# Optimization experiments

Measured on AMD Instinct MI355X. Metric: run time of the kernel, lower is better.

Reference implementation:

```python
import jax, jax.numpy as jnp
import numpy as np

BATCH, INPUTDIM, OUTDIM, GRIDSIZE = 4096, 256, 256, 64


def setup_inputs() -> dict:
    key = jax.random.key(0)
    k1, k2 = jax.random.split(key)
    x = jax.random.normal(k1, (BATCH, INPUTDIM), dtype=jnp.float32)
    # xavier_uniform over (2, outdim, inputdim, gridsize): fan_in = inputdim*gridsize, fan_out = outdim*gridsize
    fan_in = INPUTDIM * GRIDSIZE
    fan_out = OUTDIM * GRIDSIZE
    limit = float(np.sqrt(6.0 / (fan_in + fan_out)))
    fouriercoeffs = jax.random.uniform(
        k2, (2, OUTDIM, INPUTDIM, GRIDSIZE), dtype=jnp.float32,
        minval=-limit, maxval=limit)
    bias = jnp.zeros((1, OUTDIM), dtype=jnp.float32)
    return {"x": x, "fouriercoeffs": fouriercoeffs, "bias": bias}


def reference(x, fouriercoeffs, bias):
    # x: [B, inputdim]; fouriercoeffs: [2, outdim, inputdim, gridsize]; bias: [1, outdim]
    # gridsize_param is clamp/round'ed to an int in torch -> static = initial_gridsize here.
    G = fouriercoeffs.shape[-1]
    k = jnp.arange(1, G + 1, dtype=x.dtype)        # [G] frequencies 1..G
    xk = x[:, :, None] * k                          # [B, inputdim, G]
    c = jnp.cos(xk)                                 # [B, inputdim, G]
    s = jnp.sin(xk)                                 # [B, inputdim, G]
    # Fused contraction over (inputdim, gridsize) -- avoids the naive
    # [B, outdim, inputdim, gridsize] broadcast tensor of the torch code.
    y = (jnp.einsum('big,oig->bo', c, fouriercoeffs[0])
         + jnp.einsum('big,oig->bo', s, fouriercoeffs[1])
         + bias)                                    # [B, outdim]
    return y
```

## Files before the change

### kernel.cpp

```cpp
#include <hip/hip_runtime.h>
#include <hip/hip_bf16.h>


typedef __attribute__((ext_vector_type(8))) short short8;
typedef __attribute__((ext_vector_type(4))) float f32x4;

#define SPLITK 8
#define ICHUNK (256 / SPLITK)

__device__ __forceinline__ unsigned short f2bf(float f) {
    unsigned u = __builtin_bit_cast(unsigned, f);
    u += 0x7fffu + ((u >> 16) & 1u);
    return (unsigned short)(u >> 16);
}
__device__ __forceinline__ unsigned pkbf16(float a, float b) {
    return (unsigned)f2bf(a) | ((unsigned)f2bf(b) << 16);
}

__device__ __forceinline__ unsigned pk_rh(float a, float b) {
    unsigned ua = __builtin_bit_cast(unsigned, a) + 0x8000u;
    unsigned ub = __builtin_bit_cast(unsigned, b) + 0x8000u;
    return __builtin_amdgcn_perm(ub, ua, 0x07060302u);
}

__device__ __forceinline__ void dbl2(float c, float s, float& co, float& so) {
    float t = c + c;
    co = __builtin_fmaf(t, c, -1.f);
    so = t * s;
}
__device__ __forceinline__ void rot2(float c, float s, float cr, float sr,
                                     float& co, float& so) {
    float t = s * sr;
    co = __builtin_fmaf(c, cr, -t);
    float u = s * cr;
    so = __builtin_fmaf(c, sr, u);
}

__device__ __forceinline__ short8 chain8(float m1, float fm1, float f0) {
    unsigned r[4];
    float vp = fm1, v = f0;
    #pragma unroll
    for (int h = 0; h < 4; ++h) {
        float v1 = __builtin_fmaf(m1, v, -vp);
        r[h] = pk_rh(v, v1);
        float v2 = __builtin_fmaf(m1, v1, -v);
        vp = v1; v = v2;
    }
    uint4 u; u.x = r[0]; u.y = r[1]; u.z = r[2]; u.w = r[3];
    return __builtin_bit_cast(short8, u);
}

__device__ __forceinline__ void async_load16(const void* g, void* l) {
    __builtin_amdgcn_global_load_lds(
        (const __attribute__((address_space(1))) unsigned int*)g,
        (__attribute__((address_space(3))) unsigned int*)l,
        16, 0, 0);
}

__global__ void init_out_kernel(float* __restrict__ out, const float* __restrict__ bias) {
    int tid = blockIdx.x * 256 + threadIdx.x;
    float4 b4 = ((const float4*)bias)[tid & 63];
    ((float4*)out)[tid] = b4;
}

__global__ __launch_bounds__(256) void convert_coeffs2(
    const float* __restrict__ fc, unsigned short* __restrict__ ws2)
{
    __shared__ unsigned short lsh[256 * 72];
    const int bx = blockIdx.x;
    const int i = bx >> 1, y = bx & 1;
    const int t = threadIdx.x;
    {
        const int tt = t >> 7, op = t & 127;
        const float4* src = (const float4*)(fc +
            ((((size_t)tt * 256) + y * 128 + op) * 256 + i) * 64);
        uint4* dst = (uint4*)(lsh + t * 72);
        #pragma unroll
        for (int q2 = 0; q2 < 8; ++q2) {
            float4 a = src[q2 * 2], b = src[q2 * 2 + 1];
            uint4 v;
            v.x = pkbf16(a.x, a.y); v.y = pkbf16(a.z, a.w);
            v.z = pkbf16(b.x, b.y); v.w = pkbf16(b.z, b.w);
            dst[q2] = v;
        }
    }
    __syncthreads();
    uint4* wdst = (uint4*)ws2 + (size_t)bx * 2048;
    #pragma unroll
    for (int rep = 0; rep < 8; ++rep) {
        int gi = rep * 256 + t;
        int sog = gi >> 6, ll = gi & 63;
        int s = sog >> 3, og = sog & 7;
        int op = og * 16 + (ll & 15);
        int k = s * 32 + ((ll >> 4) * 8);
        int tt = k >> 6, g0 = k & 63;
        wdst[gi] = *(const uint4*)(lsh + (tt * 128 + op) * 72 + g0);
    }
}

template <bool USE_WS>
__global__ __launch_bounds__(256, 2) void fkan_gemm(
    const float* __restrict__ x, const float* __restrict__ fc,
    const unsigned short* __restrict__ bws, float* __restrict__ out)
{
    __shared__ uint4 Bimg[2][2048];
    __shared__ float xs[ICHUNK][128];

    const int t  = threadIdx.x;
    const int l  = t & 63;
    const int w  = t >> 6;
    const int wr = w >> 1, wc = w & 1;
    const int q  = l >> 4;
    const int m  = l & 15;
    const int rowBase = blockIdx.x * 128;
    const int by      = blockIdx.y;
    const int colBase = by * 128;
    const int iBase   = blockIdx.z * ICHUNK;
    const float q8f   = (float)(q * 8);

    f32x4 acc[4][4];
    #pragma unroll
    for (int a = 0; a < 4; ++a)
        #pragma unroll
        for (int b = 0; b < 4; ++b) acc[a][b] = (f32x4)0.0f;

    auto stageB = [&](int p, int i) {
        if (USE_WS) {
            const unsigned short* base = bws + ((size_t)(i * 2 + by) * 2048) * 8;
            #pragma unroll
            for (int cc = 0; cc < 8; ++cc) {
                int c = cc * 4 + w;
                async_load16(base + (size_t)(c * 64 + l) * 8, (void*)(&Bimg[p][c * 64]));
            }
        } else {
            #pragma unroll
            for (int gg = 0; gg < 8; ++gg) {
                int gi  = gg * 256 + t;
                int sog = gi >> 6, ll = gi & 63;
                int s = sog >> 3, ogb = sog & 7;
                int o = ogb * 16 + (ll & 15);
                int k = s * 32 + (ll >> 4) * 8;
                int tt = k >> 6, g = k & 63;
                const float4* p4 = (const float4*)(fc +
                    ((((size_t)tt * 256 + colBase + o) * 256 + i) * 64 + g));
                float4 a = p4[0], b = p4[1];
                uint4 v;
                v.x = pkbf16(a.x, a.y); v.y = pkbf16(a.z, a.w);
                v.z = pkbf16(b.x, b.y); v.w = pkbf16(b.z, b.w);
                Bimg[p][gi] = v;
            }
        }
    };

    stageB(0, iBase);
    {
        int r = t >> 1, c0 = (t & 1) * 16;
        const float4* px = (const float4*)(x + (size_t)(rowBase + r) * 256 + iBase + c0);
        float4 v0 = px[0], v1 = px[1], v2 = px[2], v3 = px[3];
        float tmp[16] = { v0.x, v0.y, v0.z, v0.w, v1.x, v1.y, v1.z, v1.w,
                          v2.x, v2.y, v2.z, v2.w, v3.x, v3.y, v3.z, v3.w };
        #pragma unroll
        for (int j = 0; j < 16; ++j) xs[c0 + j][r] = tmp[j];
    }
    __syncthreads();

    #pragma unroll 1
    for (int ii = 0; ii < ICHUNK; ++ii) {
        const int p = ii & 1;

        short8 bF[4][4];
        #pragma unroll
        for (int s = 0; s < 4; ++s)
            #pragma unroll
            for (int cf = 0; cf < 4; ++cf)
                bF[s][cf] = __builtin_bit_cast(short8,
                    Bimg[p][(s * 8 + wc * 4 + cf) * 64 + l]);

        if (ii + 1 < ICHUNK) stageB(p ^ 1, iBase + ii + 1);

        short8 aF[4][4];
        #pragma unroll
        for (int rf = 0; rf < 4; ++rf) {
            float xv = xs[ii][wr * 64 + rf * 16 + m];
            float s1, c1;
            __sincosf(xv, &s1, &c1);
            const float m1 = c1 + c1;
            float c2, s2, c4, s4, c8, s8, c16, s16, c32, s32;
            dbl2(c1, s1, c2, s2);
            dbl2(c2, s2, c4, s4);
            dbl2(c4, s4, c8, s8);
            dbl2(c8, s8, c16, s16);
            dbl2(c16, s16, c32, s32);
            float c24, s24;
            rot2(c16, s16, c8, s8, c24, s24);
            float cq = (q == 0) ? 1.f : (q == 1) ? c8 : (q == 2) ? c16 : c24;
            float sq = (q == 0) ? 0.f : (q == 1) ? s8 : (q == 2) ? s16 : s24;
            float cq1, sq1, cB, sB, cB1, sB1;
            rot2(cq, sq, c1, s1, cq1, sq1);
            rot2(cq, sq, c32, s32, cB, sB);
            rot2(cB, sB, c1, s1, cB1, sB1);
            aF[rf][0] = chain8(m1, cq, cq1);
            aF[rf][1] = chain8(m1, cB, cB1);
            aF[rf][2] = chain8(m1, sq, sq1);
            aF[rf][3] = chain8(m1, sB, sB1);
        }

        #pragma unroll
        for (int s = 0; s < 4; ++s)
            #pragma unroll
            for (int rf = 0; rf < 4; ++rf)
                #pragma unroll
                for (int cf = 0; cf < 4; ++cf)
                    acc[rf][cf] = __builtin_amdgcn_mfma_f32_16x16x32_bf16(
                        aF[rf][s], bF[s][cf], acc[rf][cf], 0, 0, 0);

        __syncthreads();
    }

    const int lr = (l >> 4) * 4;
    const int r0 = rowBase + wr * 64 + lr;
    const int c0 = colBase + wc * 64 + m;
    #pragma unroll
    for (int rf = 0; rf < 4; ++rf)
        #pragma unroll
        for (int cf = 0; cf < 4; ++cf)
            #pragma unroll
            for (int e = 0; e < 4; ++e)
                atomicAdd(out + (size_t)(r0 + rf * 16 + e) * 256 + (c0 + cf * 16),
                          acc[rf][cf][e]);
}

extern "C" void kernel_launch(void* const* d_in, const int* in_sizes, int n_in,
                              void* d_out, int out_size, void* d_ws, size_t ws_size,
                              hipStream_t stream) {
    const float* x    = (const float*)d_in[0];
    const float* fc   = (const float*)d_in[1];
    const float* bias = (const float*)d_in[2];
    float* out = (float*)d_out;
    unsigned short* bws = (unsigned short*)d_ws;

    hipLaunchKernelGGL(init_out_kernel, dim3(1024), dim3(256), 0, stream, out, bias);

    const size_t wsNeed = (size_t)512 * 2048 * 16;
    if (ws_size >= wsNeed) {
        hipLaunchKernelGGL(convert_coeffs2, dim3(512), dim3(256), 0, stream, fc, bws);
        hipLaunchKernelGGL((fkan_gemm<true>), dim3(32, 2, SPLITK), dim3(256), 0, stream,
                           x, fc, bws, out);
    } else {
        hipLaunchKernelGGL((fkan_gemm<false>), dim3(32, 2, SPLITK), dim3(256), 0, stream,
                           x, fc, bws, out);
    }
}
```

Baseline: 182.7 us.

## Simplify coefficient conversion, use hardware bf16 packing and native sin/cos

The coefficient conversion kernel is rewritten to drop its LDS staging. Each thread now reads its 8 floats straight from global memory at the target layout, converts them and writes one 16-byte packed value, using 8x more blocks. bf16 packing uses the hardware cvt_pk_bf16_f32 builtin when available, which gives round-to-nearest-even instead of the previous round-half-up trick. In the main GEMM, __sincosf is replaced with the native v_sin/v_cos builtins on x/(2π), which drops range reduction and risks accuracy for large |x|. The strided global reads in conversion may coalesce worse than the previous staged version.

```diff
diff --git a/kernel.cpp b/kernel.cpp
--- a/kernel.cpp
+++ b/kernel.cpp
@@ -8,20 +8,21 @@
 #define SPLITK 8
 #define ICHUNK (256 / SPLITK)
 
-__device__ __forceinline__ unsigned short f2bf(float f) {
-    unsigned u = __builtin_bit_cast(unsigned, f);
-    u += 0x7fffu + ((u >> 16) & 1u);
-    return (unsigned short)(u >> 16);
-}
+#define INV2PI 0.15915494309189535f
+
+#if __has_builtin(__builtin_amdgcn_cvt_pk_bf16_f32)
+typedef __attribute__((ext_vector_type(2))) __bf16 bf16x2_t;
 __device__ __forceinline__ unsigned pkbf16(float a, float b) {
-    return (unsigned)f2bf(a) | ((unsigned)f2bf(b) << 16);
-}
-
-__device__ __forceinline__ unsigned pk_rh(float a, float b) {
+    bf16x2_t v = __builtin_amdgcn_cvt_pk_bf16_f32(a, b);
+    return __builtin_bit_cast(unsigned, v);
+}
+#else
+__device__ __forceinline__ unsigned pkbf16(float a, float b) {
     unsigned ua = __builtin_bit_cast(unsigned, a) + 0x8000u;
     unsigned ub = __builtin_bit_cast(unsigned, b) + 0x8000u;
     return __builtin_amdgcn_perm(ub, ua, 0x07060302u);
 }
+#endif
 
 __device__ __forceinline__ void dbl2(float c, float s, float& co, float& so) {
     float t = c + c;
@@ -42,7 +43,7 @@
     #pragma unroll
     for (int h = 0; h < 4; ++h) {
         float v1 = __builtin_fmaf(m1, v, -vp);
-        r[h] = pk_rh(v, v1);
+        r[h] = pkbf16(v, v1);
         float v2 = __builtin_fmaf(m1, v1, -v);
         vp = v1; v = v2;
     }
@@ -63,39 +64,24 @@
     ((float4*)out)[tid] = b4;
 }
 
-__global__ __launch_bounds__(256) void convert_coeffs2(
+__global__ __launch_bounds__(256) void convert_coeffs3(
     const float* __restrict__ fc, unsigned short* __restrict__ ws2)
 {
-    __shared__ unsigned short lsh[256 * 72];
-    const int bx = blockIdx.x;
-    const int i = bx >> 1, y = bx & 1;
-    const int t = threadIdx.x;
-    {
-        const int tt = t >> 7, op = t & 127;
-        const float4* src = (const float4*)(fc +
-            ((((size_t)tt * 256) + y * 128 + op) * 256 + i) * 64);
-        uint4* dst = (uint4*)(lsh + t * 72);
-        #pragma unroll
-        for (int q2 = 0; q2 < 8; ++q2) {
-            float4 a = src[q2 * 2], b = src[q2 * 2 + 1];
-            uint4 v;
-            v.x = pkbf16(a.x, a.y); v.y = pkbf16(a.z, a.w);
-            v.z = pkbf16(b.x, b.y); v.w = pkbf16(b.z, b.w);
-            dst[q2] = v;
-        }
-    }
-    __syncthreads();
-    uint4* wdst = (uint4*)ws2 + (size_t)bx * 2048;
-    #pragma unroll
-    for (int rep = 0; rep < 8; ++rep) {
-        int gi = rep * 256 + t;
-        int sog = gi >> 6, ll = gi & 63;
-        int s = sog >> 3, og = sog & 7;
-        int op = og * 16 + (ll & 15);
-        int k = s * 32 + ((ll >> 4) * 8);
-        int tt = k >> 6, g0 = k & 63;
-        wdst[gi] = *(const uint4*)(lsh + (tt * 128 + op) * 72 + g0);
-    }
+    unsigned flat = blockIdx.x * 256 + threadIdx.x;
+    unsigned bx = flat >> 11, gi = flat & 2047;
+    unsigned i = bx >> 1, y = bx & 1;
+    unsigned sog = gi >> 6, ll = gi & 63;
+    unsigned s = sog >> 3, og = sog & 7;
+    unsigned op = og * 16 + (ll & 15);
+    unsigned k = s * 32 + ((ll >> 4) * 8);
+    unsigned tt = k >> 6, g0 = k & 63;
+    const float4* src = (const float4*)(fc +
+        ((((size_t)tt * 256 + y * 128 + op) * 256 + i) * 64 + g0));
+    float4 a = src[0], b = src[1];
+    uint4 v;
+    v.x = pkbf16(a.x, a.y); v.y = pkbf16(a.z, a.w);
+    v.z = pkbf16(b.x, b.y); v.w = pkbf16(b.z, b.w);
+    ((uint4*)ws2)[flat] = v;
 }
 
 template <bool USE_WS>
@@ -116,7 +102,6 @@
     const int by      = blockIdx.y;
     const int colBase = by * 128;
     const int iBase   = blockIdx.z * ICHUNK;
-    const float q8f   = (float)(q * 8);
 
     f32x4 acc[4][4];
     #pragma unroll
@@ -182,8 +167,9 @@
         #pragma unroll
         for (int rf = 0; rf < 4; ++rf) {
             float xv = xs[ii][wr * 64 + rf * 16 + m];
-            float s1, c1;
-            __sincosf(xv, &s1, &c1);
+            float rev = xv * INV2PI;
+            float s1 = __builtin_amdgcn_sinf(rev);
+            float c1 = __builtin_amdgcn_cosf(rev);
             const float m1 = c1 + c1;
             float c2, s2, c4, s4, c8, s8, c16, s16, c32, s32;
             dbl2(c1, s1, c2, s2);
@@ -243,7 +229,7 @@
 
     const size_t wsNeed = (size_t)512 * 2048 * 16;
     if (ws_size >= wsNeed) {
-        hipLaunchKernelGGL(convert_coeffs2, dim3(512), dim3(256), 0, stream, fc, bws);
+        hipLaunchKernelGGL(convert_coeffs3, dim3(4096), dim3(256), 0, stream, fc, bws);
         hipLaunchKernelGGL((fkan_gemm<true>), dim3(32, 2, SPLITK), dim3(256), 0, stream,
                            x, fc, bws, out);
     } else {
```

Result: no change. 181.5 us (-0.6%).
